# Kernel optimization log

Hardware: AMD Instinct MI355X
Metric: run time of the kernel (lower is better)

Reference implementation:

```python
import jax, jax.numpy as jnp
import numpy as np

B, S, H = 2, 1024, 1024
NH, NKV, HD = 16, 4, 64
E, K, I = 8, 2, 3584
EPS = 1e-5
THETA = 1e6


def setup_inputs() -> dict:
    key = jax.random.key(0)
    ks = jax.random.split(key, 12)
    sc = 0.02
    return {
        "hidden_states": jax.random.normal(ks[0], (B, S, H), jnp.float32),
        "ln1_w": jnp.ones((H,), jnp.float32),
        "wq": jax.random.normal(ks[1], (H, NH * HD), jnp.float32) * sc,
        "wk": jax.random.normal(ks[2], (H, NKV * HD), jnp.float32) * sc,
        "wv": jax.random.normal(ks[3], (H, NKV * HD), jnp.float32) * sc,
        "wo": jax.random.normal(ks[4], (NH * HD, H), jnp.float32) * sc,
        "ln2_w": jnp.ones((H,), jnp.float32),
        "router_w": jax.random.normal(ks[5], (H, E), jnp.float32) * sc,
        "w_gate": jax.random.normal(ks[6], (E, H, I), jnp.float32) * sc,
        "w_up": jax.random.normal(ks[7], (E, H, I), jnp.float32) * sc,
        "w_down": jax.random.normal(ks[8], (E, I, H), jnp.float32) * sc,
    }


def _rmsnorm(x, w):
    xf = x.astype(jnp.float32)
    return (xf * jax.lax.rsqrt(jnp.mean(xf * xf, axis=-1, keepdims=True) + EPS)).astype(x.dtype) * w


def _rope_cos_sin():
    inv_freq = 1.0 / (THETA ** (jnp.arange(0, HD, 2, dtype=jnp.float32) / HD))
    ang = jnp.arange(S, dtype=jnp.float32)[:, None] * inv_freq[None, :]  # [S, HD//2]
    emb = jnp.concatenate([ang, ang], axis=-1)  # [S, HD]
    return jnp.cos(emb)[None, :, None, :], jnp.sin(emb)[None, :, None, :]


def _rotate_half(x):
    return jnp.concatenate([-x[..., HD // 2:], x[..., : HD // 2]], axis=-1)


def _attention(x, wq, wk, wv, wo):
    q = (x @ wq).reshape(B, S, NH, HD)
    k = (x @ wk).reshape(B, S, NKV, HD)
    v = (x @ wv).reshape(B, S, NKV, HD)
    cos, sin = _rope_cos_sin()
    q = q * cos + _rotate_half(q) * sin
    k = k * cos + _rotate_half(k) * sin
    rep = NH // NKV
    k = jnp.repeat(k, rep, axis=2)  # [B,S,NH,HD]
    v = jnp.repeat(v, rep, axis=2)
    scores = jnp.einsum("bqhd,bkhd->bhqk", q, k) / jnp.sqrt(jnp.float32(HD))
    causal = jnp.tril(jnp.ones((S, S), bool))
    scores = jnp.where(causal[None, None], scores, jnp.float32(-1e9))
    probs = jax.nn.softmax(scores, axis=-1)
    out = jnp.einsum("bhqk,bkhd->bqhd", probs, v).reshape(B, S, NH * HD)
    return out @ wo


def _moe(x, router_w, w_gate, w_up, w_down):
    t = x.reshape(B * S, H)  # [T,H]
    logits = t @ router_w  # [T,E]
    probs = jax.nn.softmax(logits.astype(jnp.float32), axis=-1)
    top_v, top_i = jax.lax.top_k(probs, K)
    top_v = top_v / jnp.sum(top_v, axis=-1, keepdims=True)  # normalize_top_k_affinities
    # dense combine weights [T,E]
    dense_w = jnp.sum(jax.nn.one_hot(top_i, E, dtype=t.dtype) * top_v[..., None], axis=1)
    out = jnp.zeros_like(t)
    for e in range(E):  # small fixed expert loop (E=8)
        g = jax.nn.silu(t @ w_gate[e]) * (t @ w_up[e])
        out = out + dense_w[:, e:e + 1] * (g @ w_down[e])
    return out.reshape(B, S, H)


def reference(hidden_states, ln1_w, wq, wk, wv, wo, ln2_w, router_w, w_gate, w_up, w_down):
    residual = hidden_states
    h = _rmsnorm(hidden_states, ln1_w)
    h = residual + _attention(h, wq, wk, wv, wo)
    residual = h
    h2 = _rmsnorm(h, ln2_w)
    h = residual + _moe(h2, router_w, w_gate, w_up, w_down)
    return h
```

## Files before the change

kernel.cpp:

```cpp
#include <hip/hip_runtime.h>
#include <hip/hip_bf16.h>
#include <math.h>

#define B_ 2
#define S_ 1024
#define H_ 1024
#define NH_ 16
#define NKV_ 4
#define HD_ 64
#define E_ 8
#define I_ 3584
#define T_ (B_*S_)

#define BM 64
#define BN 64
#define BK 32
#define MBM 128
#define DBM 64
#define MBK 64

typedef __bf16 bf16x8 __attribute__((ext_vector_type(8)));
typedef float f32x4 __attribute__((ext_vector_type(4)));

__device__ __forceinline__ __bf16 bf_hi(float f) { return (__bf16)f; }
__device__ __forceinline__ __bf16 bf_lo(float f, __bf16 h) { return (__bf16)(f - (float)h); }

__device__ __forceinline__ int swz(int row, int col) {
    return (row * 64 + col * 2) ^ (((row >> 3) & 7) << 4);
}
__device__ __forceinline__ int swz128(int row, int col) {
    return (row * 128 + col * 2) ^ ((row & 7) << 4);
}

__global__ __launch_bounds__(256) void cvt_bf16_kernel(
    const float* __restrict__ src, __bf16* __restrict__ dst, int n8)
{
    int idx = blockIdx.x * 256 + threadIdx.x;
    if (idx >= n8) return;
    const float4* s = (const float4*)src + (size_t)idx * 2;
    float4 a = s[0], b = s[1];
    bf16x8 v;
    v[0] = (__bf16)a.x; v[1] = (__bf16)a.y; v[2] = (__bf16)a.z; v[3] = (__bf16)a.w;
    v[4] = (__bf16)b.x; v[5] = (__bf16)b.y; v[6] = (__bf16)b.z; v[7] = (__bf16)b.w;
    ((bf16x8*)dst)[idx] = v;
}

__global__ __launch_bounds__(256) void split_bf16_kernel(
    const float* __restrict__ src, __bf16* __restrict__ hi, __bf16* __restrict__ lo,
    float scale, int n8)
{
    int idx = blockIdx.x * 256 + threadIdx.x;
    if (idx >= n8) return;
    const float4* s = (const float4*)src + (size_t)idx * 2;
    float4 a = s[0], b = s[1];
    float f[8] = {a.x, a.y, a.z, a.w, b.x, b.y, b.z, b.w};
    bf16x8 vh, vl;
#pragma unroll
    for (int i = 0; i < 8; i++) {
        float x = f[i] * scale;
        __bf16 h = bf_hi(x);
        vh[i] = h;
        vl[i] = bf_lo(x, h);
    }
    ((bf16x8*)hi)[idx] = vh;
    ((bf16x8*)lo)[idx] = vl;
}

__global__ __launch_bounds__(256) void transpose_cvt_kernel(
    const float* __restrict__ src, __bf16* __restrict__ dst, int M, int N)
{
    int e = blockIdx.z;
    src += (size_t)e * M * N;
    dst += (size_t)e * M * N;
    int n0 = blockIdx.x * 64, m0 = blockIdx.y * 64;
    __shared__ __bf16 Ts[64][72];
    int tid = threadIdx.x;
#pragma unroll
    for (int i = 0; i < 16; i++) {
        int row = i * 4 + (tid >> 6);
        int col = tid & 63;
        Ts[row][col] = (__bf16)src[(size_t)(m0 + row) * N + n0 + col];
    }
    __syncthreads();
#pragma unroll
    for (int j = 0; j < 2; j++) {
        int n = (tid >> 3) + j * 32;
        int k8 = (tid & 7) * 8;
        bf16x8 v;
#pragma unroll
        for (int ii = 0; ii < 8; ii++) v[ii] = Ts[k8 + ii][n];
        *(bf16x8*)(dst + (size_t)(n0 + n) * M + m0 + k8) = v;
    }
}

__global__ __launch_bounds__(256) void rmsnorm_kernel(
    const float* __restrict__ x, const float* __restrict__ w, float* __restrict__ out)
{
    int row = blockIdx.x;
    int tid = threadIdx.x;
    const float* xr = x + (size_t)row * H_;
    float vals[4];
    float ss = 0.f;
#pragma unroll
    for (int i = 0; i < 4; i++) {
        vals[i] = xr[tid + 256 * i];
        ss += vals[i] * vals[i];
    }
#pragma unroll
    for (int off = 32; off; off >>= 1) ss += __shfl_xor(ss, off);
    __shared__ float red[4];
    int wid = tid >> 6;
    if ((tid & 63) == 0) red[wid] = ss;
    __syncthreads();
    float tot = red[0] + red[1] + red[2] + red[3];
    float scale = rsqrtf(tot * (1.0f / H_) + 1e-5f);
#pragma unroll
    for (int i = 0; i < 4; i++)
        out[(size_t)row * H_ + tid + 256 * i] = vals[i] * scale * w[tid + 256 * i];
}

__global__ __launch_bounds__(256) void gemm_bf16(
    const float* __restrict__ A, const float* __restrict__ Bm,
    float* __restrict__ C, const float* __restrict__ res,
    int M, int N, int Kd)
{
    __shared__ __bf16 As[BM * BK];
    __shared__ __bf16 Bs[BN * BK];
    char* Asb = (char*)As;
    char* Bsb = (char*)Bs;
    int tid = threadIdx.x;
    int lane = tid & 63, wid = tid >> 6;
    int wm = wid >> 1, wn = wid & 1;
    int m0 = blockIdx.y * BM, n0 = blockIdx.x * BN;
    f32x4 acc[2][2] = {};
    int ar = tid >> 2, ac = (tid & 3) * 8;
    int bk = tid >> 3, bc = (tid & 7) * 8;
    for (int kt = 0; kt < Kd; kt += BK) {
        const float* ag = A + (size_t)(m0 + ar) * Kd + kt + ac;
        bf16x8 av;
#pragma unroll
        for (int i = 0; i < 8; i++) av[i] = (__bf16)ag[i];
        *(bf16x8*)(Asb + swz(ar, ac)) = av;
        const float* bg = Bm + (size_t)(kt + bk) * N + n0 + bc;
#pragma unroll
        for (int i = 0; i < 8; i++)
            *(__bf16*)(Bsb + swz(bc + i, bk)) = (__bf16)bg[i];
        __syncthreads();
        int r = lane & 15, k8 = (lane >> 4) * 8;
        bf16x8 af[2], bfr[2];
#pragma unroll
        for (int m = 0; m < 2; m++) af[m] = *(const bf16x8*)(Asb + swz(wm * 32 + m * 16 + r, k8));
#pragma unroll
        for (int n = 0; n < 2; n++) bfr[n] = *(const bf16x8*)(Bsb + swz(wn * 32 + n * 16 + r, k8));
#pragma unroll
        for (int m = 0; m < 2; m++)
#pragma unroll
            for (int n = 0; n < 2; n++)
                acc[m][n] = __builtin_amdgcn_mfma_f32_16x16x32_bf16(af[m], bfr[n], acc[m][n], 0, 0, 0);
        __syncthreads();
    }
    int cl = lane & 15, rb = (lane >> 4) * 4;
#pragma unroll
    for (int m = 0; m < 2; m++)
#pragma unroll
        for (int n = 0; n < 2; n++)
#pragma unroll
            for (int j = 0; j < 4; j++) {
                int row = m0 + wm * 32 + m * 16 + rb + j;
                int col = n0 + wn * 32 + n * 16 + cl;
                size_t o = (size_t)row * N + col;
                float v = acc[m][n][j];
                if (res) v += res[o];
                C[o] = v;
            }
}

__global__ void rope_kernel(float* __restrict__ x, int heads, int total)
{
    int idx = blockIdx.x * blockDim.x + threadIdx.x;
    if (idx >= total) return;
    int j = idx & 31;
    int th = idx >> 5;
    int h = th % heads;
    int t = th / heads;
    int s = t & (S_ - 1);
    float inv = powf(1e6f, -(float)j / 32.0f);
    float ang = (float)s * inv;
    float c = cosf(ang), sn = sinf(ang);
    size_t base = (size_t)t * heads * HD_ + (size_t)h * HD_;
    float x1 = x[base + j], x2 = x[base + 32 + j];
    x[base + j] = x1 * c - x2 * sn;
    x[base + 32 + j] = x2 * c + x1 * sn;
}

#define LP 72
__global__ __launch_bounds__(256) void flash_kernel(
    const __bf16* __restrict__ qhi, const __bf16* __restrict__ qlo_g,
    const __bf16* __restrict__ khi, const __bf16* __restrict__ klo,
    const __bf16* __restrict__ vhi, const __bf16* __restrict__ vlo,
    float* __restrict__ o)
{
    __shared__ __bf16 Ks [64][LP];
    __shared__ __bf16 Ksl[64][LP];
    __shared__ __bf16 Vt [64][LP];
    __shared__ __bf16 Vtl[64][LP];
    __shared__ __bf16 Pl [4][16][LP];
    __shared__ __bf16 Pll[4][16][LP];

    int tid = threadIdx.x;
    int lane = tid & 63, wid = tid >> 6;
    int qr = lane & 15, quad = lane >> 4;
    int qt = (S_ / 16 - 1) - blockIdx.x;
    int kvh = blockIdx.y, b = blockIdx.z;
    int h = kvh * 4 + wid;
    int s0 = qt * 16;

    size_t qoff = ((size_t)(b * S_ + s0 + qr) * NH_ + h) * HD_ + quad * 8;
    bf16x8 qf[2], qlo[2];
#pragma unroll
    for (int ks = 0; ks < 2; ks++) {
        qf[ks]  = *(const bf16x8*)(qhi  + qoff + ks * 32);
        qlo[ks] = *(const bf16x8*)(qlo_g + qoff + ks * 32);
    }

    float m_run[4], l_run[4];
    f32x4 o_acc[4] = {};
#pragma unroll
    for (int j = 0; j < 4; j++) { m_run[j] = -1e30f; l_run[j] = 0.f; }

    int skey = tid >> 2, shd0 = (tid & 3) * 16;
    int vhd = tid & 63, vkey0 = (tid >> 6) * 16;

    for (int kt = 0; kt <= s0 + 15; kt += 64) {
        __syncthreads();
        {
            size_t koff = ((size_t)(b * S_ + kt + skey) * NKV_ + kvh) * HD_ + shd0;
            *(bf16x8*)&Ks [skey][shd0]     = *(const bf16x8*)(khi + koff);
            *(bf16x8*)&Ks [skey][shd0 + 8] = *(const bf16x8*)(khi + koff + 8);
            *(bf16x8*)&Ksl[skey][shd0]     = *(const bf16x8*)(klo + koff);
            *(bf16x8*)&Ksl[skey][shd0 + 8] = *(const bf16x8*)(klo + koff + 8);
        }
        {
            const __bf16* vh = vhi + ((size_t)(b * S_ + kt + vkey0) * NKV_ + kvh) * HD_ + vhd;
            const __bf16* vl = vlo + ((size_t)(b * S_ + kt + vkey0) * NKV_ + kvh) * HD_ + vhd;
            bf16x8 th0, th1, tl0, tl1;
#pragma unroll
            for (int i = 0; i < 8; i++) {
                th0[i] = vh[(size_t)i * (NKV_ * HD_)];
                th1[i] = vh[(size_t)(i + 8) * (NKV_ * HD_)];
                tl0[i] = vl[(size_t)i * (NKV_ * HD_)];
                tl1[i] = vl[(size_t)(i + 8) * (NKV_ * HD_)];
            }
            *(bf16x8*)&Vt [vhd][vkey0]     = th0;
            *(bf16x8*)&Vt [vhd][vkey0 + 8] = th1;
            *(bf16x8*)&Vtl[vhd][vkey0]     = tl0;
            *(bf16x8*)&Vtl[vhd][vkey0 + 8] = tl1;
        }
        __syncthreads();

        f32x4 sc4[4];
#pragma unroll
        for (int sub = 0; sub < 4; sub++) {
            int krow = sub * 16 + qr;
            bf16x8 kh0 = *(const bf16x8*)&Ks [krow][quad * 8];
            bf16x8 kh1 = *(const bf16x8*)&Ks [krow][32 + quad * 8];
            bf16x8 kl0 = *(const bf16x8*)&Ksl[krow][quad * 8];
            bf16x8 kl1 = *(const bf16x8*)&Ksl[krow][32 + quad * 8];
            f32x4 z = {};
            z = __builtin_amdgcn_mfma_f32_16x16x32_bf16(qf[0],  kh0, z, 0, 0, 0);
            z = __builtin_amdgcn_mfma_f32_16x16x32_bf16(qf[1],  kh1, z, 0, 0, 0);
            z = __builtin_amdgcn_mfma_f32_16x16x32_bf16(qlo[0], kh0, z, 0, 0, 0);
            z = __builtin_amdgcn_mfma_f32_16x16x32_bf16(qlo[1], kh1, z, 0, 0, 0);
            z = __builtin_amdgcn_mfma_f32_16x16x32_bf16(qf[0],  kl0, z, 0, 0, 0);
            z = __builtin_amdgcn_mfma_f32_16x16x32_bf16(qf[1],  kl1, z, 0, 0, 0);
            sc4[sub] = z;
        }
        if (kt + 63 > s0) {
#pragma unroll
            for (int sub = 0; sub < 4; sub++)
#pragma unroll
                for (int j = 0; j < 4; j++) {
                    int key = kt + sub * 16 + qr;
                    int row = s0 + quad * 4 + j;
                    if (key > row) sc4[sub][j] = -1e30f;
                }
        }
#pragma unroll
        for (int j = 0; j < 4; j++) {
            float mx = fmaxf(fmaxf(sc4[0][j], sc4[1][j]), fmaxf(sc4[2][j], sc4[3][j]));
#pragma unroll
            for (int off = 1; off < 16; off <<= 1) mx = fmaxf(mx, __shfl_xor(mx, off));
            float mn = fmaxf(m_run[j], mx);
            float scale = __expf(m_run[j] - mn);
            m_run[j] = mn;
            float rs = 0.f;
#pragma unroll
            for (int sub = 0; sub < 4; sub++) {
                float pe = __expf(sc4[sub][j] - mn);
                sc4[sub][j] = pe;
                rs += pe;
            }
#pragma unroll
            for (int off = 1; off < 16; off <<= 1) rs += __shfl_xor(rs, off);
            l_run[j] = l_run[j] * scale + rs;
#pragma unroll
            for (int sub = 0; sub < 4; sub++) o_acc[sub][j] *= scale;
        }
#pragma unroll
        for (int sub = 0; sub < 4; sub++)
#pragma unroll
            for (int j = 0; j < 4; j++) {
                float pe = sc4[sub][j];
                __bf16 hh = bf_hi(pe);
                Pl [wid][quad * 4 + j][sub * 16 + qr] = hh;
                Pll[wid][quad * 4 + j][sub * 16 + qr] = bf_lo(pe, hh);
            }
        __syncthreads();
        bf16x8 ph0 = *(const bf16x8*)&Pl [wid][qr][quad * 8];
        bf16x8 ph1 = *(const bf16x8*)&Pl [wid][qr][32 + quad * 8];
        bf16x8 pl0 = *(const bf16x8*)&Pll[wid][qr][quad * 8];
        bf16x8 pl1 = *(const bf16x8*)&Pll[wid][qr][32 + quad * 8];
#pragma unroll
        for (int sub = 0; sub < 4; sub++) {
            int vrow = sub * 16 + qr;
            bf16x8 vh0 = *(const bf16x8*)&Vt [vrow][quad * 8];
            bf16x8 vh1 = *(const bf16x8*)&Vt [vrow][32 + quad * 8];
            bf16x8 vl0 = *(const bf16x8*)&Vtl[vrow][quad * 8];
            bf16x8 vl1 = *(const bf16x8*)&Vtl[vrow][32 + quad * 8];
            o_acc[sub] = __builtin_amdgcn_mfma_f32_16x16x32_bf16(ph0, vh0, o_acc[sub], 0, 0, 0);
            o_acc[sub] = __builtin_amdgcn_mfma_f32_16x16x32_bf16(ph1, vh1, o_acc[sub], 0, 0, 0);
            o_acc[sub] = __builtin_amdgcn_mfma_f32_16x16x32_bf16(ph0, vl0, o_acc[sub], 0, 0, 0);
            o_acc[sub] = __builtin_amdgcn_mfma_f32_16x16x32_bf16(ph1, vl1, o_acc[sub], 0, 0, 0);
            o_acc[sub] = __builtin_amdgcn_mfma_f32_16x16x32_bf16(pl0, vh0, o_acc[sub], 0, 0, 0);
            o_acc[sub] = __builtin_amdgcn_mfma_f32_16x16x32_bf16(pl1, vh1, o_acc[sub], 0, 0, 0);
        }
    }
#pragma unroll
    for (int j = 0; j < 4; j++) {
        float inv = 1.f / l_run[j];
        int row = s0 + quad * 4 + j;
#pragma unroll
        for (int sub = 0; sub < 4; sub++)
            o[((size_t)(b * S_ + row) * NH_ + h) * HD_ + sub * 16 + qr] = o_acc[sub][j] * inv;
    }
}

__global__ __launch_bounds__(256) void router_kernel(
    const float* __restrict__ xn, const float* __restrict__ rw,
    int* __restrict__ top_i, float* __restrict__ top_w)
{
    int wid = threadIdx.x >> 6, lane = threadIdx.x & 63;
    int t = blockIdx.x * 4 + wid;
    const float* xr = xn + (size_t)t * H_;
    float acc[E_] = {};
    for (int c = 0; c < H_ / 64; c++) {
        float xd = xr[c * 64 + lane];
        const float* wrow = rw + (size_t)(c * 64 + lane) * E_;
#pragma unroll
        for (int e = 0; e < E_; e++) acc[e] += xd * wrow[e];
    }
#pragma unroll
    for (int e = 0; e < E_; e++) {
        float r = acc[e];
#pragma unroll
        for (int off = 32; off; off >>= 1) r += __shfl_xor(r, off);
        acc[e] = r;
    }
    if (lane == 0) {
        float mx = acc[0];
        for (int e = 1; e < E_; e++) mx = fmaxf(mx, acc[e]);
        float p[E_], sum = 0.f;
        for (int e = 0; e < E_; e++) { p[e] = __expf(acc[e] - mx); sum += p[e]; }
        float inv_s = 1.f / sum;
        for (int e = 0; e < E_; e++) p[e] *= inv_s;
        int i0 = 0;
        for (int e = 1; e < E_; e++) if (p[e] > p[i0]) i0 = e;
        int i1 = (i0 == 0) ? 1 : 0;
        for (int e = 0; e < E_; e++) if (e != i0 && p[e] > p[i1]) i1 = e;
        float v0 = p[i0], v1 = p[i1], inv = 1.f / (v0 + v1);
        top_i[t * 2] = i0; top_i[t * 2 + 1] = i1;
        top_w[t * 2] = v0 * inv; top_w[t * 2 + 1] = v1 * inv;
    }
}

__global__ void assign_kernel(
    const int* __restrict__ top_i, const float* __restrict__ top_w,
    int* __restrict__ tlist, int* __restrict__ pair_pos,
    int* __restrict__ counts, int* __restrict__ offsets)
{
    __shared__ int cnt[E_], off[E_], fill[E_];
    int tid = threadIdx.x;
    if (tid < E_) { cnt[tid] = 0; fill[tid] = 0; }
    __syncthreads();
    for (int t = tid; t < T_; t += 256) {
        atomicAdd(&cnt[top_i[t * 2]], 1);
        atomicAdd(&cnt[top_i[t * 2 + 1]], 1);
    }
    __syncthreads();
    if (tid == 0) {
        int o = 0;
        for (int e = 0; e < E_; e++) { off[e] = o; o += cnt[e]; }
    }
    __syncthreads();
    for (int t = tid; t < T_; t += 256) {
        for (int j = 0; j < 2; j++) {
            int e = top_i[t * 2 + j];
            int pos = off[e] + atomicAdd(&fill[e], 1);
            tlist[pos] = t;
            pair_pos[t * 2 + j] = pos;
        }
    }
    __syncthreads();
    if (tid < E_) { counts[tid] = cnt[tid]; offsets[tid] = off[tid]; }
}

__global__ __launch_bounds__(256) void moe_gemm_gateup(
    const __bf16* __restrict__ Xb, const __bf16* __restrict__ WgT, const __bf16* __restrict__ WuT,
    __bf16* __restrict__ act, const int* __restrict__ tlist,
    const int* __restrict__ counts, const int* __restrict__ offsets)
{
    int e = blockIdx.z;
    int cnt = counts[e], off = offsets[e];
    int m0 = blockIdx.y * MBM;
    if (m0 >= cnt) return;
    int n0 = blockIdx.x * BN;
    const __bf16* Bg = WgT + (size_t)e * H_ * I_;
    const __bf16* Bu = WuT + (size_t)e * H_ * I_;
    __shared__ __bf16 As[2][MBM * MBK];
    __shared__ __bf16 Gs[2][BN * MBK];
    __shared__ __bf16 Us[2][BN * MBK];
    __shared__ int rowidx[MBM];
    int tid = threadIdx.x;
    if (tid < MBM) {
        int rl = m0 + tid;
        rowidx[tid] = tlist[off + ((rl < cnt) ? rl : 0)];
    }
    __syncthreads();
    int lane = tid & 63, wid = tid >> 6;
    f32x4 accg[2][4] = {}, accu[2][4] = {};
    int ar = tid >> 1, ac = (tid & 1) * 32;
    int bn = tid >> 2, bc = (tid & 3) * 16;
    const __bf16* abase = Xb + (size_t)rowidx[ar] * H_ + ac;
    const __bf16* gbase = Bg + (size_t)(n0 + bn) * H_ + bc;
    const __bf16* ubase = Bu + (size_t)(n0 + bn) * H_ + bc;
    {
        char* Asb = (char*)As[0];
        char* Gsb = (char*)Gs[0];
        char* Usb = (char*)Us[0];
#pragma unroll
        for (int g = 0; g < 4; g++)
            *(bf16x8*)(Asb + swz128(ar, ac + g * 8)) = *(const bf16x8*)(abase + g * 8);
#pragma unroll
        for (int g = 0; g < 2; g++) {
            *(bf16x8*)(Gsb + swz128(bn, bc + g * 8)) = *(const bf16x8*)(gbase + g * 8);
            *(bf16x8*)(Usb + swz128(bn, bc + g * 8)) = *(const bf16x8*)(ubase + g * 8);
        }
    }
    bf16x8 pa[4], pg[2], pu[2];
    if (H_ > MBK) {
#pragma unroll
        for (int g = 0; g < 4; g++) pa[g] = *(const bf16x8*)(abase + MBK + g * 8);
#pragma unroll
        for (int g = 0; g < 2; g++) {
            pg[g] = *(const bf16x8*)(gbase + MBK + g * 8);
            pu[g] = *(const bf16x8*)(ubase + MBK + g * 8);
        }
    }
    int cur = 0;
    int r = lane & 15, q8 = (lane >> 4) * 8;
    for (int kt = 0; kt < H_; kt += MBK) {
        __syncthreads();
        char* Asb = (char*)As[cur];
        char* Gsb = (char*)Gs[cur];
        char* Usb = (char*)Us[cur];
#pragma unroll
        for (int kk = 0; kk < 2; kk++) {
            bf16x8 af[2], gf[4], uf[4];
#pragma unroll
            for (int m = 0; m < 2; m++)
                af[m] = *(const bf16x8*)(Asb + swz128(wid * 32 + m * 16 + r, kk * 32 + q8));
#pragma unroll
            for (int n = 0; n < 4; n++) {
                gf[n] = *(const bf16x8*)(Gsb + swz128(n * 16 + r, kk * 32 + q8));
                uf[n] = *(const bf16x8*)(Usb + swz128(n * 16 + r, kk * 32 + q8));
            }
#pragma unroll
            for (int m = 0; m < 2; m++)
#pragma unroll
                for (int n = 0; n < 4; n++) {
                    accg[m][n] = __builtin_amdgcn_mfma_f32_16x16x32_bf16(af[m], gf[n], accg[m][n], 0, 0, 0);
                    accu[m][n] = __builtin_amdgcn_mfma_f32_16x16x32_bf16(af[m], uf[n], accu[m][n], 0, 0, 0);
                }
        }
        int kn = kt + MBK;
        if (kn < H_) {
            char* Asw = (char*)As[cur ^ 1];
            char* Gsw = (char*)Gs[cur ^ 1];
            char* Usw = (char*)Us[cur ^ 1];
#pragma unroll
            for (int g = 0; g < 4; g++) *(bf16x8*)(Asw + swz128(ar, ac + g * 8)) = pa[g];
#pragma unroll
            for (int g = 0; g < 2; g++) {
                *(bf16x8*)(Gsw + swz128(bn, bc + g * 8)) = pg[g];
                *(bf16x8*)(Usw + swz128(bn, bc + g * 8)) = pu[g];
            }
            int k2 = kn + MBK;
            if (k2 < H_) {
#pragma unroll
                for (int g = 0; g < 4; g++) pa[g] = *(const bf16x8*)(abase + k2 + g * 8);
#pragma unroll
                for (int g = 0; g < 2; g++) {
                    pg[g] = *(const bf16x8*)(gbase + k2 + g * 8);
                    pu[g] = *(const bf16x8*)(ubase + k2 + g * 8);
                }
            }
            cur ^= 1;
        }
    }
    int cl = lane & 15, rb = (lane >> 4) * 4;
#pragma unroll
    for (int m = 0; m < 2; m++)
#pragma unroll
        for (int n = 0; n < 4; n++)
#pragma unroll
            for (int j = 0; j < 4; j++) {
                int rl = m0 + wid * 32 + m * 16 + rb + j;
                if (rl >= cnt) continue;
                int col = n0 + n * 16 + cl;
                float g = accg[m][n][j], u = accu[m][n][j];
                float sig = 1.f / (1.f + __expf(-g));
                act[(size_t)(off + rl) * I_ + col] = (__bf16)(g * sig * u);
            }
}

__global__ __launch_bounds__(256) void moe_gemm_down(
    const __bf16* __restrict__ act, const __bf16* __restrict__ WdT,
    float* __restrict__ dout, const int* __restrict__ counts, const int* __restrict__ offsets)
{
    int e = blockIdx.z;
    int cnt = counts[e], off = offsets[e];
    int m0 = blockIdx.y * DBM;
    if (m0 >= cnt) return;
    int n0 = blockIdx.x * BN;
    const __bf16* Bw = WdT + (size_t)e * I_ * H_;
    __shared__ __bf16 As[2][DBM * MBK];
    __shared__ __bf16 Bs[2][BN * MBK];
    int tid = threadIdx.x;
    int lane = tid & 63, wid = tid >> 6;
    f32x4 acc[4] = {};
    int ar = tid >> 2, ac = (tid & 3) * 16;
    int bn = tid >> 2, bc = (tid & 3) * 16;
    int arow = m0 + ar; if (arow >= cnt) arow = cnt - 1;
    const __bf16* abase = act + (size_t)(off + arow) * I_ + ac;
    const __bf16* bbase = Bw + (size_t)(n0 + bn) * I_ + bc;
    {
        char* Asb = (char*)As[0];
        char* Bsb = (char*)Bs[0];
#pragma unroll
        for (int g = 0; g < 2; g++) {
            *(bf16x8*)(Asb + swz128(ar, ac + g * 8)) = *(const bf16x8*)(abase + g * 8);
            *(bf16x8*)(Bsb + swz128(bn, bc + g * 8)) = *(const bf16x8*)(bbase + g * 8);
        }
    }
    bf16x8 pa[2], pb[2];
    if (I_ > MBK) {
#pragma unroll
        for (int g = 0; g < 2; g++) {
            pa[g] = *(const bf16x8*)(abase + MBK + g * 8);
            pb[g] = *(const bf16x8*)(bbase + MBK + g * 8);
        }
    }
    int cur = 0;
    int r = lane & 15, q8 = (lane >> 4) * 8;
    for (int kt = 0; kt < I_; kt += MBK) {
        __syncthreads();
        char* Asb = (char*)As[cur];
        char* Bsb = (char*)Bs[cur];
#pragma unroll
        for (int kk = 0; kk < 2; kk++) {
            bf16x8 af = *(const bf16x8*)(Asb + swz128(wid * 16 + r, kk * 32 + q8));
            bf16x8 bfr[4];
#pragma unroll
            for (int n = 0; n < 4; n++)
                bfr[n] = *(const bf16x8*)(Bsb + swz128(n * 16 + r, kk * 32 + q8));
#pragma unroll
            for (int n = 0; n < 4; n++)
                acc[n] = __builtin_amdgcn_mfma_f32_16x16x32_bf16(af, bfr[n], acc[n], 0, 0, 0);
        }
        int kn = kt + MBK;
        if (kn < I_) {
            char* Asw = (char*)As[cur ^ 1];
            char* Bsw = (char*)Bs[cur ^ 1];
#pragma unroll
            for (int g = 0; g < 2; g++) {
                *(bf16x8*)(Asw + swz128(ar, ac + g * 8)) = pa[g];
                *(bf16x8*)(Bsw + swz128(bn, bc + g * 8)) = pb[g];
            }
            int k2 = kn + MBK;
            if (k2 < I_) {
#pragma unroll
                for (int g = 0; g < 2; g++) {
                    pa[g] = *(const bf16x8*)(abase + k2 + g * 8);
                    pb[g] = *(const bf16x8*)(bbase + k2 + g * 8);
                }
            }
            cur ^= 1;
        }
    }
    int cl = lane & 15, rb = (lane >> 4) * 4;
#pragma unroll
    for (int n = 0; n < 4; n++)
#pragma unroll
        for (int j = 0; j < 4; j++) {
            int rl = m0 + wid * 16 + rb + j;
            if (rl >= cnt) continue;
            int col = n0 + n * 16 + cl;
            dout[(size_t)(off + rl) * H_ + col] = acc[n][j];
        }
}

__global__ __launch_bounds__(256) void combine_kernel(
    const float* __restrict__ hres, const float* __restrict__ dout,
    const int* __restrict__ pair_pos, const float* __restrict__ top_w,
    float* __restrict__ out)
{
    int idx = blockIdx.x * 256 + threadIdx.x;
    int t = idx >> 10, d = idx & 1023;
    float v = hres[idx];
    int p0 = pair_pos[t * 2], p1 = pair_pos[t * 2 + 1];
    v += top_w[t * 2] * dout[(size_t)p0 * H_ + d]
       + top_w[t * 2 + 1] * dout[(size_t)p1 * H_ + d];
    out[idx] = v;
}

extern "C" void kernel_launch(void* const* d_in, const int* in_sizes, int n_in,
                              void* d_out, int out_size, void* d_ws, size_t ws_size,
                              hipStream_t stream) {
    const float* hidden = (const float*)d_in[0];
    const float* ln1 = (const float*)d_in[1];
    const float* wq = (const float*)d_in[2];
    const float* wk = (const float*)d_in[3];
    const float* wv = (const float*)d_in[4];
    const float* wo = (const float*)d_in[5];
    const float* ln2 = (const float*)d_in[6];
    const float* rw = (const float*)d_in[7];
    const float* wg = (const float*)d_in[8];
    const float* wu = (const float*)d_in[9];
    const float* wd = (const float*)d_in[10];
    float* out = (float*)d_out;

    char* ws = (char*)d_ws;
    size_t o = 0;
    auto alloc = [&](size_t bytes) -> void* {
        void* p = ws + o;
        o += (bytes + 255) & ~(size_t)255;
        return p;
    };
    float* xn   = (float*)alloc((size_t)T_ * H_ * 4);
    float* qb   = (float*)alloc((size_t)T_ * NH_ * HD_ * 4);
    float* kb   = (float*)alloc((size_t)T_ * NKV_ * HD_ * 4);
    float* vb   = (float*)alloc((size_t)T_ * NKV_ * HD_ * 4);
    float* attn = (float*)alloc((size_t)T_ * H_ * 4);
    float* hres = (float*)alloc((size_t)T_ * H_ * 4);
    int*   top_i    = (int*)alloc((size_t)T_ * 2 * 4);
    float* top_w    = (float*)alloc((size_t)T_ * 2 * 4);
    int*   pair_pos = (int*)alloc((size_t)T_ * 2 * 4);
    int*   tlist    = (int*)alloc((size_t)T_ * 2 * 4);
    int*   counts   = (int*)alloc(E_ * 4);
    int*   offsets  = (int*)alloc(E_ * 4);
    __bf16* actb  = (__bf16*)alloc((size_t)T_ * 2 * I_ * 2);
    float*  doutb = (float*)alloc((size_t)T_ * 2 * H_ * 4);
    __bf16* xnb = (__bf16*)alloc((size_t)T_ * H_ * 2);
    __bf16* wgt = (__bf16*)alloc((size_t)E_ * H_ * I_ * 2);
    __bf16* wut = (__bf16*)alloc((size_t)E_ * H_ * I_ * 2);
    __bf16* wdt = (__bf16*)alloc((size_t)E_ * I_ * H_ * 2);
    __bf16* qhib = (__bf16*)alloc((size_t)T_ * NH_ * HD_ * 2);
    __bf16* qlob = (__bf16*)alloc((size_t)T_ * NH_ * HD_ * 2);
    __bf16* khib = (__bf16*)alloc((size_t)T_ * NKV_ * HD_ * 2);
    __bf16* klob = (__bf16*)alloc((size_t)T_ * NKV_ * HD_ * 2);
    __bf16* vhib = (__bf16*)alloc((size_t)T_ * NKV_ * HD_ * 2);
    __bf16* vlob = (__bf16*)alloc((size_t)T_ * NKV_ * HD_ * 2);

    transpose_cvt_kernel<<<dim3(I_ / 64, H_ / 64, E_), 256, 0, stream>>>(wg, wgt, H_, I_);
    transpose_cvt_kernel<<<dim3(I_ / 64, H_ / 64, E_), 256, 0, stream>>>(wu, wut, H_, I_);
    transpose_cvt_kernel<<<dim3(H_ / 64, I_ / 64, E_), 256, 0, stream>>>(wd, wdt, I_, H_);

    rmsnorm_kernel<<<T_, 256, 0, stream>>>(hidden, ln1, xn);
    gemm_bf16<<<dim3((NH_ * HD_) / BN, T_ / BM), 256, 0, stream>>>(xn, wq, qb, nullptr, T_, NH_ * HD_, H_);
    gemm_bf16<<<dim3((NKV_ * HD_) / BN, T_ / BM), 256, 0, stream>>>(xn, wk, kb, nullptr, T_, NKV_ * HD_, H_);
    gemm_bf16<<<dim3((NKV_ * HD_) / BN, T_ / BM), 256, 0, stream>>>(xn, wv, vb, nullptr, T_, NKV_ * HD_, H_);
    {
        int tq = T_ * NH_ * 32, tk = T_ * NKV_ * 32;
        rope_kernel<<<(tq + 255) / 256, 256, 0, stream>>>(qb, NH_, tq);
        rope_kernel<<<(tk + 255) / 256, 256, 0, stream>>>(kb, NKV_, tk);
    }
    {
        int nq8 = T_ * NH_ * HD_ / 8, nk8 = T_ * NKV_ * HD_ / 8;
        split_bf16_kernel<<<(nq8 + 255) / 256, 256, 0, stream>>>(qb, qhib, qlob, 0.125f, nq8);
        split_bf16_kernel<<<(nk8 + 255) / 256, 256, 0, stream>>>(kb, khib, klob, 1.0f, nk8);
        split_bf16_kernel<<<(nk8 + 255) / 256, 256, 0, stream>>>(vb, vhib, vlob, 1.0f, nk8);
    }
    flash_kernel<<<dim3(S_ / 16, NKV_, B_), 256, 0, stream>>>(qhib, qlob, khib, klob, vhib, vlob, attn);
    gemm_bf16<<<dim3(H_ / BN, T_ / BM), 256, 0, stream>>>(attn, wo, hres, hidden, T_, H_, H_);
    rmsnorm_kernel<<<T_, 256, 0, stream>>>(hres, ln2, xn);
    cvt_bf16_kernel<<<(T_ * H_ / 8 + 255) / 256, 256, 0, stream>>>(xn, xnb, T_ * H_ / 8);
    router_kernel<<<T_ / 4, 256, 0, stream>>>(xn, rw, top_i, top_w);
    assign_kernel<<<1, 256, 0, stream>>>(top_i, top_w, tlist, pair_pos, counts, offsets);
    moe_gemm_gateup<<<dim3(I_ / BN, T_ / MBM, E_), 256, 0, stream>>>(xnb, wgt, wut, actb, tlist, counts, offsets);
    moe_gemm_down<<<dim3(H_ / BN, T_ / DBM, E_), 256, 0, stream>>>(actb, wdt, doutb, counts, offsets);
    combine_kernel<<<(T_ * H_) / 256, 256, 0, stream>>>(hres, doutb, pair_pos, top_w, out);
}
```

Measured before the change: 498.8 us.

## Use pre-transposed bf16 weights and double-buffered GEMM for attention projections; fuse rope+split

Attention projection GEMMs now read bf16 activations and pre-transposed bf16 weights with 128-bit loads, a 64-wide K tile and LDS double buffering, replacing per-element fp32 loads and conversions. RMSNorm writes bf16 directly, which removes the separate convert kernel. RoPE is fused with the hi/lo bf16 split, and the flash kernel writes bf16 output, cutting fp32 round trips. Four extra transpose kernels run each call to prepare the weights, and the attention output loses precision by being stored in bf16.

```diff
diff --git a/kernel.cpp b/kernel.cpp
--- a/kernel.cpp
+++ b/kernel.cpp
@@ -14,7 +14,6 @@
 
 #define BM 64
 #define BN 64
-#define BK 32
 #define MBM 128
 #define DBM 64
 #define MBK 64
@@ -25,24 +24,8 @@
 __device__ __forceinline__ __bf16 bf_hi(float f) { return (__bf16)f; }
 __device__ __forceinline__ __bf16 bf_lo(float f, __bf16 h) { return (__bf16)(f - (float)h); }
 
-__device__ __forceinline__ int swz(int row, int col) {
-    return (row * 64 + col * 2) ^ (((row >> 3) & 7) << 4);
-}
 __device__ __forceinline__ int swz128(int row, int col) {
     return (row * 128 + col * 2) ^ ((row & 7) << 4);
-}
-
-__global__ __launch_bounds__(256) void cvt_bf16_kernel(
-    const float* __restrict__ src, __bf16* __restrict__ dst, int n8)
-{
-    int idx = blockIdx.x * 256 + threadIdx.x;
-    if (idx >= n8) return;
-    const float4* s = (const float4*)src + (size_t)idx * 2;
-    float4 a = s[0], b = s[1];
-    bf16x8 v;
-    v[0] = (__bf16)a.x; v[1] = (__bf16)a.y; v[2] = (__bf16)a.z; v[3] = (__bf16)a.w;
-    v[4] = (__bf16)b.x; v[5] = (__bf16)b.y; v[6] = (__bf16)b.z; v[7] = (__bf16)b.w;
-    ((bf16x8*)dst)[idx] = v;
 }
 
 __global__ __launch_bounds__(256) void split_bf16_kernel(
@@ -94,7 +77,8 @@
 }
 
 __global__ __launch_bounds__(256) void rmsnorm_kernel(
-    const float* __restrict__ x, const float* __restrict__ w, float* __restrict__ out)
+    const float* __restrict__ x, const float* __restrict__ w,
+    __bf16* __restrict__ outb, float* __restrict__ outf)
 {
     int row = blockIdx.x;
     int tid = threadIdx.x;
@@ -115,67 +99,100 @@
     float tot = red[0] + red[1] + red[2] + red[3];
     float scale = rsqrtf(tot * (1.0f / H_) + 1e-5f);
 #pragma unroll
-    for (int i = 0; i < 4; i++)
-        out[(size_t)row * H_ + tid + 256 * i] = vals[i] * scale * w[tid + 256 * i];
-}
-
-__global__ __launch_bounds__(256) void gemm_bf16(
-    const float* __restrict__ A, const float* __restrict__ Bm,
+    for (int i = 0; i < 4; i++) {
+        float y = vals[i] * scale * w[tid + 256 * i];
+        outb[(size_t)row * H_ + tid + 256 * i] = (__bf16)y;
+        if (outf) outf[(size_t)row * H_ + tid + 256 * i] = y;
+    }
+}
+
+__global__ __launch_bounds__(256) void gemm_bf16bt(
+    const __bf16* __restrict__ A, const __bf16* __restrict__ BT,
     float* __restrict__ C, const float* __restrict__ res,
     int M, int N, int Kd)
 {
-    __shared__ __bf16 As[BM * BK];
-    __shared__ __bf16 Bs[BN * BK];
-    char* Asb = (char*)As;
-    char* Bsb = (char*)Bs;
+    int m0 = blockIdx.y * DBM;
+    int n0 = blockIdx.x * BN;
+    __shared__ __bf16 As[2][DBM * MBK];
+    __shared__ __bf16 Bs[2][BN * MBK];
     int tid = threadIdx.x;
     int lane = tid & 63, wid = tid >> 6;
-    int wm = wid >> 1, wn = wid & 1;
-    int m0 = blockIdx.y * BM, n0 = blockIdx.x * BN;
-    f32x4 acc[2][2] = {};
-    int ar = tid >> 2, ac = (tid & 3) * 8;
-    int bk = tid >> 3, bc = (tid & 7) * 8;
-    for (int kt = 0; kt < Kd; kt += BK) {
-        const float* ag = A + (size_t)(m0 + ar) * Kd + kt + ac;
-        bf16x8 av;
-#pragma unroll
-        for (int i = 0; i < 8; i++) av[i] = (__bf16)ag[i];
-        *(bf16x8*)(Asb + swz(ar, ac)) = av;
-        const float* bg = Bm + (size_t)(kt + bk) * N + n0 + bc;
-#pragma unroll
-        for (int i = 0; i < 8; i++)
-            *(__bf16*)(Bsb + swz(bc + i, bk)) = (__bf16)bg[i];
+    f32x4 acc[4] = {};
+    int ar = tid >> 2, ac = (tid & 3) * 16;
+    int bn = tid >> 2, bc = (tid & 3) * 16;
+    const __bf16* abase = A + (size_t)(m0 + ar) * Kd + ac;
+    const __bf16* bbase = BT + (size_t)(n0 + bn) * Kd + bc;
+    {
+        char* Asb = (char*)As[0];
+        char* Bsb = (char*)Bs[0];
+#pragma unroll
+        for (int g = 0; g < 2; g++) {
+            *(bf16x8*)(Asb + swz128(ar, ac + g * 8)) = *(const bf16x8*)(abase + g * 8);
+            *(bf16x8*)(Bsb + swz128(bn, bc + g * 8)) = *(const bf16x8*)(bbase + g * 8);
+        }
+    }
+    bf16x8 pa[2], pb[2];
+    if (Kd > MBK) {
+#pragma unroll
+        for (int g = 0; g < 2; g++) {
+            pa[g] = *(const bf16x8*)(abase + MBK + g * 8);
+            pb[g] = *(const bf16x8*)(bbase + MBK + g * 8);
+        }
+    }
+    int cur = 0;
+    int r = lane & 15, q8 = (lane >> 4) * 8;
+    for (int kt = 0; kt < Kd; kt += MBK) {
         __syncthreads();
-        int r = lane & 15, k8 = (lane >> 4) * 8;
-        bf16x8 af[2], bfr[2];
-#pragma unroll
-        for (int m = 0; m < 2; m++) af[m] = *(const bf16x8*)(Asb + swz(wm * 32 + m * 16 + r, k8));
-#pragma unroll
-        for (int n = 0; n < 2; n++) bfr[n] = *(const bf16x8*)(Bsb + swz(wn * 32 + n * 16 + r, k8));
-#pragma unroll
-        for (int m = 0; m < 2; m++)
-#pragma unroll
-            for (int n = 0; n < 2; n++)
-                acc[m][n] = __builtin_amdgcn_mfma_f32_16x16x32_bf16(af[m], bfr[n], acc[m][n], 0, 0, 0);
-        __syncthreads();
+        char* Asb = (char*)As[cur];
+        char* Bsb = (char*)Bs[cur];
+#pragma unroll
+        for (int kk = 0; kk < 2; kk++) {
+            bf16x8 af = *(const bf16x8*)(Asb + swz128(wid * 16 + r, kk * 32 + q8));
+            bf16x8 bfr[4];
+#pragma unroll
+            for (int n = 0; n < 4; n++)
+                bfr[n] = *(const bf16x8*)(Bsb + swz128(n * 16 + r, kk * 32 + q8));
+#pragma unroll
+            for (int n = 0; n < 4; n++)
+                acc[n] = __builtin_amdgcn_mfma_f32_16x16x32_bf16(af, bfr[n], acc[n], 0, 0, 0);
+        }
+        int kn = kt + MBK;
+        if (kn < Kd) {
+            char* Asw = (char*)As[cur ^ 1];
+            char* Bsw = (char*)Bs[cur ^ 1];
+#pragma unroll
+            for (int g = 0; g < 2; g++) {
+                *(bf16x8*)(Asw + swz128(ar, ac + g * 8)) = pa[g];
+                *(bf16x8*)(Bsw + swz128(bn, bc + g * 8)) = pb[g];
+            }
+            int k2 = kn + MBK;
+            if (k2 < Kd) {
+#pragma unroll
+                for (int g = 0; g < 2; g++) {
+                    pa[g] = *(const bf16x8*)(abase + k2 + g * 8);
+                    pb[g] = *(const bf16x8*)(bbase + k2 + g * 8);
+                }
+            }
+            cur ^= 1;
+        }
     }
     int cl = lane & 15, rb = (lane >> 4) * 4;
 #pragma unroll
-    for (int m = 0; m < 2; m++)
-#pragma unroll
-        for (int n = 0; n < 2; n++)
-#pragma unroll
-            for (int j = 0; j < 4; j++) {
-                int row = m0 + wm * 32 + m * 16 + rb + j;
-                int col = n0 + wn * 32 + n * 16 + cl;
-                size_t o = (size_t)row * N + col;
-                float v = acc[m][n][j];
-                if (res) v += res[o];
-                C[o] = v;
-            }
-}
-
-__global__ void rope_kernel(float* __restrict__ x, int heads, int total)
+    for (int n = 0; n < 4; n++)
+#pragma unroll
+        for (int j = 0; j < 4; j++) {
+            int row = m0 + wid * 16 + rb + j;
+            int col = n0 + n * 16 + cl;
+            size_t o = (size_t)row * N + col;
+            float v = acc[n][j];
+            if (res) v += res[o];
+            C[o] = v;
+        }
+}
+
+__global__ void rope_split_kernel(
+    const float* __restrict__ x, __bf16* __restrict__ hi, __bf16* __restrict__ lo,
+    float scale, int heads, int total)
 {
     int idx = blockIdx.x * blockDim.x + threadIdx.x;
     if (idx >= total) return;
@@ -189,8 +206,11 @@
     float c = cosf(ang), sn = sinf(ang);
     size_t base = (size_t)t * heads * HD_ + (size_t)h * HD_;
     float x1 = x[base + j], x2 = x[base + 32 + j];
-    x[base + j] = x1 * c - x2 * sn;
-    x[base + 32 + j] = x2 * c + x1 * sn;
+    float y1 = (x1 * c - x2 * sn) * scale;
+    float y2 = (x2 * c + x1 * sn) * scale;
+    __bf16 h1 = bf_hi(y1), h2 = bf_hi(y2);
+    hi[base + j] = h1;       lo[base + j] = bf_lo(y1, h1);
+    hi[base + 32 + j] = h2;  lo[base + 32 + j] = bf_lo(y2, h2);
 }
 
 #define LP 72
@@ -198,7 +218,7 @@
     const __bf16* __restrict__ qhi, const __bf16* __restrict__ qlo_g,
     const __bf16* __restrict__ khi, const __bf16* __restrict__ klo,
     const __bf16* __restrict__ vhi, const __bf16* __restrict__ vlo,
-    float* __restrict__ o)
+    __bf16* __restrict__ o)
 {
     __shared__ __bf16 Ks [64][LP];
     __shared__ __bf16 Ksl[64][LP];
@@ -341,7 +361,7 @@
         int row = s0 + quad * 4 + j;
 #pragma unroll
         for (int sub = 0; sub < 4; sub++)
-            o[((size_t)(b * S_ + row) * NH_ + h) * HD_ + sub * 16 + qr] = o_acc[sub][j] * inv;
+            o[((size_t)(b * S_ + row) * NH_ + h) * HD_ + sub * 16 + qr] = (__bf16)(o_acc[sub][j] * inv);
     }
 }
 
@@ -660,7 +680,6 @@
     float* qb   = (float*)alloc((size_t)T_ * NH_ * HD_ * 4);
     float* kb   = (float*)alloc((size_t)T_ * NKV_ * HD_ * 4);
     float* vb   = (float*)alloc((size_t)T_ * NKV_ * HD_ * 4);
-    float* attn = (float*)alloc((size_t)T_ * H_ * 4);
     float* hres = (float*)alloc((size_t)T_ * H_ * 4);
     int*   top_i    = (int*)alloc((size_t)T_ * 2 * 4);
     float* top_w    = (float*)alloc((size_t)T_ * 2 * 4);
@@ -670,10 +689,16 @@
     int*   offsets  = (int*)alloc(E_ * 4);
     __bf16* actb  = (__bf16*)alloc((size_t)T_ * 2 * I_ * 2);
     float*  doutb = (float*)alloc((size_t)T_ * 2 * H_ * 4);
-    __bf16* xnb = (__bf16*)alloc((size_t)T_ * H_ * 2);
+    __bf16* xnb1 = (__bf16*)alloc((size_t)T_ * H_ * 2);
+    __bf16* xnb  = (__bf16*)alloc((size_t)T_ * H_ * 2);
+    __bf16* attnb = (__bf16*)alloc((size_t)T_ * H_ * 2);
     __bf16* wgt = (__bf16*)alloc((size_t)E_ * H_ * I_ * 2);
     __bf16* wut = (__bf16*)alloc((size_t)E_ * H_ * I_ * 2);
     __bf16* wdt = (__bf16*)alloc((size_t)E_ * I_ * H_ * 2);
+    __bf16* wqt = (__bf16*)alloc((size_t)H_ * NH_ * HD_ * 2);
+    __bf16* wkt = (__bf16*)alloc((size_t)H_ * NKV_ * HD_ * 2);
+    __bf16* wvt = (__bf16*)alloc((size_t)H_ * NKV_ * HD_ * 2);
+    __bf16* wot = (__bf16*)alloc((size_t)NH_ * HD_ * H_ * 2);
     __bf16* qhib = (__bf16*)alloc((size_t)T_ * NH_ * HD_ * 2);
     __bf16* qlob = (__bf16*)alloc((size_t)T_ * NH_ * HD_ * 2);
     __bf16* khib = (__bf16*)alloc((size_t)T_ * NKV_ * HD_ * 2);
@@ -684,26 +709,25 @@
     transpose_cvt_kernel<<<dim3(I_ / 64, H_ / 64, E_), 256, 0, stream>>>(wg, wgt, H_, I_);
     transpose_cvt_kernel<<<dim3(I_ / 64, H_ / 64, E_), 256, 0, stream>>>(wu, wut, H_, I_);
     transpose_cvt_kernel<<<dim3(H_ / 64, I_ / 64, E_), 256, 0, stream>>>(wd, wdt, I_, H_);
-
-    rmsnorm_kernel<<<T_, 256, 0, stream>>>(hidden, ln1, xn);
-    gemm_bf16<<<dim3((NH_ * HD_) / BN, T_ / BM), 256, 0, stream>>>(xn, wq, qb, nullptr, T_, NH_ * HD_, H_);
-    gemm_bf16<<<dim3((NKV_ * HD_) / BN, T_ / BM), 256, 0, stream>>>(xn, wk, kb, nullptr, T_, NKV_ * HD_, H_);
-    gemm_bf16<<<dim3((NKV_ * HD_) / BN, T_ / BM), 256, 0, stream>>>(xn, wv, vb, nullptr, T_, NKV_ * HD_, H_);
+    transpose_cvt_kernel<<<dim3((NH_ * HD_) / 64, H_ / 64, 1), 256, 0, stream>>>(wq, wqt, H_, NH_ * HD_);
+    transpose_cvt_kernel<<<dim3((NKV_ * HD_) / 64, H_ / 64, 1), 256, 0, stream>>>(wk, wkt, H_, NKV_ * HD_);
+    transpose_cvt_kernel<<<dim3((NKV_ * HD_) / 64, H_ / 64, 1), 256, 0, stream>>>(wv, wvt, H_, NKV_ * HD_);
+    transpose_cvt_kernel<<<dim3(H_ / 64, (NH_ * HD_) / 64, 1), 256, 0, stream>>>(wo, wot, NH_ * HD_, H_);
+
+    rmsnorm_kernel<<<T_, 256, 0, stream>>>(hidden, ln1, xnb1, nullptr);
+    gemm_bf16bt<<<dim3((NH_ * HD_) / BN, T_ / DBM), 256, 0, stream>>>(xnb1, wqt, qb, nullptr, T_, NH_ * HD_, H_);
+    gemm_bf16bt<<<dim3((NKV_ * HD_) / BN, T_ / DBM), 256, 0, stream>>>(xnb1, wkt, kb, nullptr, T_, NKV_ * HD_, H_);
+    gemm_bf16bt<<<dim3((NKV_ * HD_) / BN, T_ / DBM), 256, 0, stream>>>(xnb1, wvt, vb, nullptr, T_, NKV_ * HD_, H_);
     {
         int tq = T_ * NH_ * 32, tk = T_ * NKV_ * 32;
-        rope_kernel<<<(tq + 255) / 256, 256, 0, stream>>>(qb, NH_, tq);
-        rope_kernel<<<(tk + 255) / 256, 256, 0, stream>>>(kb, NKV_, tk);
-    }
-    {
-        int nq8 = T_ * NH_ * HD_ / 8, nk8 = T_ * NKV_ * HD_ / 8;
-        split_bf16_kernel<<<(nq8 + 255) / 256, 256, 0, stream>>>(qb, qhib, qlob, 0.125f, nq8);
-        split_bf16_kernel<<<(nk8 + 255) / 256, 256, 0, stream>>>(kb, khib, klob, 1.0f, nk8);
+        rope_split_kernel<<<(tq + 255) / 256, 256, 0, stream>>>(qb, qhib, qlob, 0.125f, NH_, tq);
+        rope_split_kernel<<<(tk + 255) / 256, 256, 0, stream>>>(kb, khib, klob, 1.0f, NKV_, tk);
+        int nk8 = T_ * NKV_ * HD_ / 8;
         split_bf16_kernel<<<(nk8 + 255) / 256, 256, 0, stream>>>(vb, vhib, vlob, 1.0f, nk8);
     }
-    flash_kernel<<<dim3(S_ / 16, NKV_, B_), 256, 0, stream>>>(qhib, qlob, khib, klob, vhib, vlob, attn);
-    gemm_bf16<<<dim3(H_ / BN, T_ / BM), 256, 0, stream>>>(attn, wo, hres, hidden, T_, H_, H_);
-    rmsnorm_kernel<<<T_, 256, 0, stream>>>(hres, ln2, xn);
-    cvt_bf16_kernel<<<(T_ * H_ / 8 + 255) / 256, 256, 0, stream>>>(xn, xnb, T_ * H_ / 8);
+    flash_kernel<<<dim3(S_ / 16, NKV_, B_), 256, 0, stream>>>(qhib, qlob, khib, klob, vhib, vlob, attnb);
+    gemm_bf16bt<<<dim3(H_ / BN, T_ / DBM), 256, 0, stream>>>(attnb, wot, hres, hidden, T_, H_, NH_ * HD_);
+    rmsnorm_kernel<<<T_, 256, 0, stream>>>(hres, ln2, xnb, xn);
     router_kernel<<<T_ / 4, 256, 0, stream>>>(xn, rw, top_i, top_w);
     assign_kernel<<<1, 256, 0, stream>>>(top_i, top_w, tlist, pair_pos, counts, offsets);
     moe_gemm_gateup<<<dim3(I_ / BN, T_ / MBM, E_), 256, 0, stream>>>(xnb, wgt, wut, actb, tlist, counts, offsets);
```

Result: faster. 431.7 us (-13.5%).
